# Optimization experiments

Measured on AMD Instinct MI355X. Metric: run time of the kernel, lower is better.

The kernel has to match this reference:

```python
import jax, jax.numpy as jnp
import numpy as np

KSIZE = 35
SIGMA = 0.3 * ((KSIZE - 1) * 0.5 - 1) + 0.8  # sigma_space == sigma_density == 5.6


def _gaussian_weight(k, sigma):
    # normalized 2D isotropic Gaussian, matching GaussianFilter.gaussian_weight
    g = jnp.arange(k, dtype=jnp.float32) - (k // 2)
    w = jnp.exp(-(g[:, None] ** 2 + g[None, :] ** 2) / (2.0 * sigma ** 2))
    return w / w.sum()


def setup_inputs() -> dict:
    key = jax.random.key(0)
    x = jax.random.uniform(key, (1, 3, 128, 128), dtype=jnp.float32)
    return {"x": x}


def reference(x):
    k = KSIZE
    pad = (k - 1) // 2
    B, C, H, W = x.shape
    xp = jnp.pad(x, ((0, 0), (0, 0), (pad, pad), (pad, pad)), mode='reflect')
    # unfold dims 2 and 3 -> patches [B, C, H, W, k, k]
    ri = jnp.arange(H)[:, None] + jnp.arange(k)[None, :]   # [H, k]
    rj = jnp.arange(W)[:, None] + jnp.arange(k)[None, :]   # [W, k]
    p = xp[:, :, ri, :]            # [B, C, H, k, W+2p]
    p = p[:, :, :, :, rj]          # [B, C, H, k, W, k]
    patches = jnp.transpose(p, (0, 1, 2, 4, 3, 5))  # [B, C, H, W, k, k]
    # density weights: channel-mean abs diff to center pixel
    dd = jnp.mean(jnp.abs(patches - x[..., None, None]), axis=1, keepdims=True)  # [B,1,H,W,k,k]
    wd = jnp.exp(-(dd ** 2) / (2.0 * SIGMA ** 2))
    wd = wd / wd.sum(axis=(-1, -2), keepdims=True)
    w = wd * _gaussian_weight(k, SIGMA)                    # [B,1,H,W,k,k]
    w_sum = w.sum(axis=(-1, -2))                           # [B,1,H,W]
    out = (w * patches).sum(axis=(-1, -2)) / w_sum         # [B,C,H,W]
    return out
```

## Files before the change

kernel.cpp:

```cpp
#include <hip/hip_runtime.h>
#include <math.h>

#define KS   35
#define PAD  17
#define H    128
#define W    128
#define TILE 4
#define LW   (TILE + KS - 1)
#define BLK  256

struct alignas(16) F4 { float c0, c1, c2, pd; };

__device__ __forceinline__ int reflect_idx(int p) {
    if (p < 0) p = -p;
    if (p >= H) p = 2 * H - 2 - p;
    return p;
}

__global__ __launch_bounds__(BLK, 4)
void bilateral_kernel(const float* __restrict__ x, float* __restrict__ out) {
    __shared__ F4 s_in[LW * LW];

    const int tid = threadIdx.x;
    const int tx0 = blockIdx.x * TILE;
    const int ty0 = blockIdx.y * TILE;

    const float LOG2E = 1.4426950408889634f;
    const float c_sp  = LOG2E / 62.72f;
    const float c_rng = LOG2E / (62.72f * 9.0f);

    for (int idx = tid; idx < LW * LW; idx += BLK) {
        int ly = idx / LW, lx = idx - ly * LW;
        int gy = reflect_idx(ty0 - PAD + ly);
        int gx = reflect_idx(tx0 - PAD + lx);
        F4 v;
        v.c0 = x[gy * W + gx];
        v.c1 = x[H * W + gy * W + gx];
        v.c2 = x[2 * H * W + gy * W + gx];
        v.pd = 0.0f;
        s_in[idx] = v;
    }
    __syncthreads();

    const int sub = tid & 15;
    const int pix = tid >> 4;
    const int px  = pix & 3, py = pix >> 2;
    const int si  = sub & 3, sj = sub >> 2;

    const F4 c = s_in[(py + PAD) * LW + (px + PAD)];

    float a   = -c_sp * (float)((si - PAD) * (si - PAD));
    float ad  = -c_sp * (float)(8 * (si - PAD) + 16);
    const float b0   = -c_sp * (float)((sj - PAD) * (sj - PAD));
    const float bd0  = -c_sp * (float)(8 * (sj - PAD) + 16);
    const float add2 = -32.0f * c_sp;

    float n0 = 0.f, n1 = 0.f, n2 = 0.f, den = 0.f;
    for (int di = si; di < KS; di += 4) {
        const F4* row = &s_in[(py + di) * LW + px];
        float g  = a + b0;
        float gd = bd0;
        for (int dj = sj; dj < KS; dj += 4) {
            F4 p = row[dj];
            float s = fabsf(p.c0 - c.c0) + fabsf(p.c1 - c.c1) + fabsf(p.c2 - c.c2);
            float w = __builtin_amdgcn_exp2f(fmaf(s * s, -c_rng, g));
            n0 = fmaf(w, p.c0, n0);
            n1 = fmaf(w, p.c1, n1);
            n2 = fmaf(w, p.c2, n2);
            den += w;
            g += gd; gd += add2;
        }
        a += ad; ad += add2;
    }

    for (int m = 1; m <= 8; m <<= 1) {
        n0  += __shfl_xor(n0, m);
        n1  += __shfl_xor(n1, m);
        n2  += __shfl_xor(n2, m);
        den += __shfl_xor(den, m);
    }

    if (sub == 0) {
        int gy = ty0 + py, gx = tx0 + px;
        float inv = 1.0f / den;
        out[(0 * H + gy) * W + gx] = n0 * inv;
        out[(1 * H + gy) * W + gx] = n1 * inv;
        out[(2 * H + gy) * W + gx] = n2 * inv;
    }
}

extern "C" void kernel_launch(void* const* d_in, const int* in_sizes, int n_in,
                              void* d_out, int out_size, void* d_ws, size_t ws_size,
                              hipStream_t stream) {
    const float* x = (const float*)d_in[0];
    float* out = (float*)d_out;
    dim3 grid(W / TILE, H / TILE);
    dim3 block(BLK);
    bilateral_kernel<<<grid, block, 0, stream>>>(x, out);
}
```

Before: 64.68 us.

## Register-block four pixels per thread to reuse loaded neighbors across outputs

Each thread now computes four output pixels spaced 4 apart in x. It loads a row of 12 neighbor values from LDS into registers once and reuses them across the four centers, which cuts LDS reads per weight evaluation. The tile becomes 16x2 with a 41x51 halo, and out-of-kernel taps are masked with a very negative exponent instead of loop bounds. The cost is many more registers (launch bounds lowered to 2), some exp work wasted on padded taps, and a wider 32-lane reduction.

```diff
diff --git a/kernel.cpp b/kernel.cpp
--- a/kernel.cpp
+++ b/kernel.cpp
@@ -5,8 +5,10 @@
 #define PAD  17
 #define H    128
 #define W    128
-#define TILE 4
-#define LW   (TILE + KS - 1)
+#define TLX  16
+#define TLY  2
+#define TW   51
+#define TH   41
 #define BLK  256
 
 struct alignas(16) F4 { float c0, c1, c2, pd; };
@@ -17,20 +19,21 @@
     return p;
 }
 
-__global__ __launch_bounds__(BLK, 4)
+__global__ __launch_bounds__(BLK, 2)
 void bilateral_kernel(const float* __restrict__ x, float* __restrict__ out) {
-    __shared__ F4 s_in[LW * LW];
+    __shared__ F4 s_in[TH * TW];
 
     const int tid = threadIdx.x;
-    const int tx0 = blockIdx.x * TILE;
-    const int ty0 = blockIdx.y * TILE;
+    const int tx0 = blockIdx.x * TLX;
+    const int ty0 = blockIdx.y * TLY;
 
-    const float LOG2E = 1.4426950408889634f;
-    const float c_sp  = LOG2E / 62.72f;
-    const float c_rng = LOG2E / (62.72f * 9.0f);
+    const float LOG2E  = 1.4426950408889634f;
+    const float c_sp   = LOG2E / 62.72f;
+    const float c_rng  = LOG2E / (62.72f * 9.0f);
+    const float NEGBIG = -1.0e30f;
 
-    for (int idx = tid; idx < LW * LW; idx += BLK) {
-        int ly = idx / LW, lx = idx - ly * LW;
+    for (int idx = tid; idx < TH * TW; idx += BLK) {
+        int ly = idx / TW, lx = idx - ly * TW;
         int gy = reflect_idx(ty0 - PAD + ly);
         int gx = reflect_idx(tx0 - PAD + lx);
         F4 v;
@@ -42,50 +45,83 @@
     }
     __syncthreads();
 
-    const int sub = tid & 15;
-    const int pix = tid >> 4;
-    const int px  = pix & 3, py = pix >> 2;
-    const int si  = sub & 3, sj = sub >> 2;
+    const int sub  = tid & 31;
+    const int si   = sub >> 2;
+    const int sj   = sub & 3;
+    const int quad = tid >> 5;
+    const int qy   = quad >> 2;
+    const int qr   = quad & 3;
 
-    const F4 c = s_in[(py + PAD) * LW + (px + PAD)];
+    F4 c[4];
+    #pragma unroll
+    for (int p = 0; p < 4; ++p)
+        c[p] = s_in[(qy + PAD) * TW + (qr + 4 * p + PAD)];
 
-    float a   = -c_sp * (float)((si - PAD) * (si - PAD));
-    float ad  = -c_sp * (float)(8 * (si - PAD) + 16);
-    const float b0   = -c_sp * (float)((sj - PAD) * (sj - PAD));
-    const float bd0  = -c_sp * (float)(8 * (sj - PAD) + 16);
-    const float add2 = -32.0f * c_sp;
-
-    float n0 = 0.f, n1 = 0.f, n2 = 0.f, den = 0.f;
-    for (int di = si; di < KS; di += 4) {
-        const F4* row = &s_in[(py + di) * LW + px];
-        float g  = a + b0;
-        float gd = bd0;
-        for (int dj = sj; dj < KS; dj += 4) {
-            F4 p = row[dj];
-            float s = fabsf(p.c0 - c.c0) + fabsf(p.c1 - c.c1) + fabsf(p.c2 - c.c2);
-            float w = __builtin_amdgcn_exp2f(fmaf(s * s, -c_rng, g));
-            n0 = fmaf(w, p.c0, n0);
-            n1 = fmaf(w, p.c1, n1);
-            n2 = fmaf(w, p.c2, n2);
-            den += w;
-            g += gd; gd += add2;
-        }
-        a += ad; ad += add2;
+    float b[9];
+    #pragma unroll
+    for (int j = 0; j < 9; ++j) {
+        int dj = sj + 4 * j;
+        float fd = (float)(dj - PAD);
+        b[j] = (dj <= 34) ? (-c_sp * fd * fd) : NEGBIG;
     }
 
-    for (int m = 1; m <= 8; m <<= 1) {
-        n0  += __shfl_xor(n0, m);
-        n1  += __shfl_xor(n1, m);
-        n2  += __shfl_xor(n2, m);
-        den += __shfl_xor(den, m);
+    float a0[4] = {0.f, 0.f, 0.f, 0.f};
+    float a1[4] = {0.f, 0.f, 0.f, 0.f};
+    float a2[4] = {0.f, 0.f, 0.f, 0.f};
+    float ad[4] = {0.f, 0.f, 0.f, 0.f};
+
+    #pragma unroll
+    for (int t = 0; t < 5; ++t) {
+        const int di = si + 8 * t;
+        float fdi = (float)(di - PAD);
+        float a = (di <= 34) ? (-c_sp * fdi * fdi) : NEGBIG;
+
+        const F4* row = &s_in[(qy + di) * TW + (qr + sj)];
+        F4 v[12];
+        #pragma unroll
+        for (int k = 0; k < 12; ++k) v[k] = row[4 * k];
+
+        float ab[9];
+        #pragma unroll
+        for (int j = 0; j < 9; ++j) ab[j] = a + b[j];
+
+        #pragma unroll
+        for (int p = 0; p < 4; ++p) {
+            #pragma unroll
+            for (int j = 0; j < 9; ++j) {
+                F4 q = v[p + j];
+                float s = fabsf(q.c0 - c[p].c0) + fabsf(q.c1 - c[p].c1)
+                        + fabsf(q.c2 - c[p].c2);
+                float w = __builtin_amdgcn_exp2f(fmaf(s * s, -c_rng, ab[j]));
+                a0[p] = fmaf(w, q.c0, a0[p]);
+                a1[p] = fmaf(w, q.c1, a1[p]);
+                a2[p] = fmaf(w, q.c2, a2[p]);
+                ad[p] += w;
+            }
+        }
+    }
+
+    #pragma unroll
+    for (int m = 1; m <= 16; m <<= 1) {
+        #pragma unroll
+        for (int p = 0; p < 4; ++p) {
+            a0[p] += __shfl_xor(a0[p], m);
+            a1[p] += __shfl_xor(a1[p], m);
+            a2[p] += __shfl_xor(a2[p], m);
+            ad[p] += __shfl_xor(ad[p], m);
+        }
     }
 
     if (sub == 0) {
-        int gy = ty0 + py, gx = tx0 + px;
-        float inv = 1.0f / den;
-        out[(0 * H + gy) * W + gx] = n0 * inv;
-        out[(1 * H + gy) * W + gx] = n1 * inv;
-        out[(2 * H + gy) * W + gx] = n2 * inv;
+        int gy = ty0 + qy;
+        #pragma unroll
+        for (int p = 0; p < 4; ++p) {
+            int gx = tx0 + qr + 4 * p;
+            float inv = 1.0f / ad[p];
+            out[(0 * H + gy) * W + gx] = a0[p] * inv;
+            out[(1 * H + gy) * W + gx] = a1[p] * inv;
+            out[(2 * H + gy) * W + gx] = a2[p] * inv;
+        }
     }
 }
 
@@ -94,7 +130,7 @@
                               hipStream_t stream) {
     const float* x = (const float*)d_in[0];
     float* out = (float*)d_out;
-    dim3 grid(W / TILE, H / TILE);
+    dim3 grid(W / TLX, H / TLY);
     dim3 block(BLK);
     bilateral_kernel<<<grid, block, 0, stream>>>(x, out);
 }
```

Result: no change. 64.18 us (-0.8%).
